# Optimization experiments

Hardware: AMD Instinct MI355X
Metric: run time of the kernel (lower is better)

Reference implementation:

```python
import jax, jax.numpy as jnp
import numpy as np

B, T, C = 8, 2048, 640

def setup_inputs() -> dict:
    key = jax.random.key(0)
    k1, k2, k3, k4 = jax.random.split(key, 4)
    s = 1.0 / np.sqrt(C)  # ~ torch Linear default init scale
    x = jax.random.normal(k1, (B, T, C), dtype=jnp.float32)
    w_q = jax.random.normal(k2, (C, C), dtype=jnp.float32) * s
    w_k = jax.random.normal(k3, (C, C), dtype=jnp.float32) * s
    w_v = jax.random.normal(k4, (C, C), dtype=jnp.float32) * s
    return {"x": x, "w_q": w_q, "w_k": w_k, "w_v": w_v}

def reference(x, w_q, w_k, w_v):
    # nn.Linear computes x @ W.T; weights here stored as (out, in) like torch.
    q = jnp.einsum('btc,oc->bto', x, w_q)
    k = jnp.einsum('btc,oc->bto', x, w_k)
    v = jnp.einsum('btc,oc->bto', x, w_v)
    scale = jnp.sqrt(jnp.asarray(C, dtype=x.dtype))  # note: full n_embd, not per-head
    scores = jnp.einsum('bqc,bkc->bqk', q, k) / scale  # [B,T,T]
    Tn = x.shape[1]
    causal = jnp.triu(jnp.ones((Tn, Tn), dtype=bool), k=1)
    scores = jnp.where(causal[None, :, :], jnp.asarray(-jnp.inf, dtype=x.dtype), scores)
    attn = jax.nn.softmax(scores, axis=-1)
    attn_out = jnp.einsum('bqk,bkc->bqc', attn, v)
    return x + attn_out
```

## Files before the change

kernel.cpp:

```cpp
#include <hip/hip_runtime.h>
#include <stdint.h>
#include <stddef.h>

#define T_SEQ 2048
#define C_DIM 640
#define N_BATCH 8

typedef __bf16 bf16x8 __attribute__((ext_vector_type(8)));
typedef float f32x4 __attribute__((ext_vector_type(4)));

__device__ __forceinline__ unsigned short f2bf(float f) {
  unsigned u = __float_as_uint(f);
  u += 0x7fffu + ((u >> 16) & 1u);
  return (unsigned short)(u >> 16);
}
__device__ __forceinline__ float bf2f(unsigned short h) {
  return __uint_as_float(((unsigned)h) << 16);
}

__device__ __forceinline__ void gll16(const unsigned short* src, unsigned short* dst) {
  __builtin_amdgcn_global_load_lds(
      (const __attribute__((address_space(1))) void*)src,
      (__attribute__((address_space(3))) void*)dst, 16, 0, 0);
}

__device__ __forceinline__ void stage_tile(const unsigned short* gbase, int ldg,
                                           unsigned short* lbuf, int wave, int lane) {
#pragma unroll
  for (int i = 0; i < 4; ++i) {
    const int o   = i * 4096 + wave * 1024 + lane * 16;
    const int row = o >> 7;
    const int cb  = o & 127;
    const int scb = cb ^ ((row & 7) << 4);
    const unsigned short* src = gbase + (size_t)row * ldg + (scb >> 1);
    unsigned short* dst = lbuf + ((i * 4096 + wave * 1024) >> 1);
    gll16(src, dst);
  }
}

__device__ __forceinline__ void tri_decode(int t, int& mi, int& ni) {
  int m = (int)((__fsqrt_rn(8.0f * (float)t + 1.0f) - 1.0f) * 0.5f);
  while ((m + 1) * (m + 2) / 2 <= t) ++m;
  while (m * (m + 1) / 2 > t) --m;
  mi = m;
  ni = t - m * (m + 1) / 2;
}

template <int MODE>
__global__ __launch_bounds__(256) void gemm_k(
    const unsigned short* __restrict__ Abase, const unsigned short* __restrict__ Bbase,
    unsigned short* __restrict__ OutB, float* __restrict__ OutF,
    const float* __restrict__ Lrow, const float* __restrict__ Xres,
    float* __restrict__ Lpart) {
  const int lin = blockIdx.x;
  int mi, ni, bz;
  if constexpr (MODE == 0) {
    const int wg = (lin & 7) * 240 + (lin >> 3);
    mi = wg / 15;
    const int t = wg % 15;
    bz = t / 5;
    ni = t % 5;
  } else if constexpr (MODE == 1) {
    const int wg = (lin & 7) * 136 + (lin >> 3);
    bz = wg / 136;
    tri_decode(wg % 136, mi, ni);
  } else {
    const int wg = (lin & 7) * 80 + (lin >> 3);
    bz = wg / 80;
    const int t = wg % 80;
    mi = 15 - t / 5;
    ni = t % 5;
  }

  __shared__ unsigned short As[2][8192];
  __shared__ unsigned short Bs[2][8192];
  const int tid = threadIdx.x;
  const int wave = tid >> 6, lane = tid & 63;
  const int wm = wave >> 1, wn = wave & 1;

  const unsigned short* Ap;
  const unsigned short* Bp;
  int ldA, ldB, ksteps;
  if constexpr (MODE == 0) {
    Ap = Abase + (size_t)mi * 128 * 640;
    Bp = Bbase + (size_t)bz * 409600 + (size_t)ni * 128 * 640;
    ldA = 640; ldB = 640; ksteps = 10;
  } else if constexpr (MODE == 1) {
    Ap = Abase + (size_t)bz * 1310720 + (size_t)mi * 128 * 640;
    Bp = Bbase + (size_t)bz * 1310720 + (size_t)ni * 128 * 640;
    ldA = 640; ldB = 640; ksteps = 10;
  } else {
    Ap = Abase + (size_t)bz * 4194304 + (size_t)mi * 128 * 2048;
    Bp = Bbase + (size_t)bz * 1310720 + (size_t)ni * 128 * 2048;
    ldA = 2048; ldB = 2048; ksteps = 2 * (mi + 1);
  }

  f32x4 acc[4][4] = {};

  stage_tile(Ap, ldA, As[0], wave, lane);
  stage_tile(Bp, ldB, Bs[0], wave, lane);
  __syncthreads();

  int cur = 0;
  for (int t = 0; t < ksteps; ++t) {
    if (t + 1 < ksteps) {
      stage_tile(Ap + (size_t)(t + 1) * 64, ldA, As[cur ^ 1], wave, lane);
      stage_tile(Bp + (size_t)(t + 1) * 64, ldB, Bs[cur ^ 1], wave, lane);
    }
#pragma unroll
    for (int kk = 0; kk < 2; ++kk) {
      bf16x8 af[4], bfr[4];
#pragma unroll
      for (int mt = 0; mt < 4; ++mt) {
        const int row = wm * 64 + mt * 16 + (lane & 15);
        const int cb  = kk * 64 + ((lane >> 4) << 4);
        af[mt] = *(const bf16x8*)&As[cur][row * 64 + ((cb ^ ((row & 7) << 4)) >> 1)];
      }
#pragma unroll
      for (int nt = 0; nt < 4; ++nt) {
        const int row = wn * 64 + nt * 16 + (lane & 15);
        const int cb  = kk * 64 + ((lane >> 4) << 4);
        bfr[nt] = *(const bf16x8*)&Bs[cur][row * 64 + ((cb ^ ((row & 7) << 4)) >> 1)];
      }
#pragma unroll
      for (int mt = 0; mt < 4; ++mt)
#pragma unroll
        for (int nt = 0; nt < 4; ++nt)
          acc[mt][nt] = __builtin_amdgcn_mfma_f32_16x16x32_bf16(af[mt], bfr[nt],
                                                                acc[mt][nt], 0, 0, 0);
    }
    __syncthreads();
    cur ^= 1;
  }

  if constexpr (MODE == 1) {
#pragma unroll
    for (int mt = 0; mt < 4; ++mt) {
      const int r0 = wm * 64 + mt * 16 + ((lane >> 4) << 2);
      const int grow = mi * 128 + r0;
      float rsum[4] = {0.f, 0.f, 0.f, 0.f};
#pragma unroll
      for (int nt = 0; nt < 4; ++nt) {
        const int gc = ni * 128 + wn * 64 + nt * 16 + (lane & 15);
        const size_t base = (size_t)bz * 4194304 + (size_t)grow * 2048 + gc;
#pragma unroll
        for (int r = 0; r < 4; ++r) {
          const float e = (gc <= grow + r) ? __expf(acc[mt][nt][r]) : 0.0f;
          OutB[base + (size_t)r * 2048] = f2bf(e);
          rsum[r] += e;
        }
      }
#pragma unroll
      for (int off = 1; off < 16; off <<= 1) {
#pragma unroll
        for (int r = 0; r < 4; ++r) rsum[r] += __shfl_xor(rsum[r], off);
      }
      if ((lane & 15) == 0) {
#pragma unroll
        for (int r = 0; r < 4; ++r)
          Lpart[((size_t)bz * 2048 + grow + r) * 32 + ni * 2 + wn] = rsum[r];
      }
    }
  } else {
#pragma unroll
    for (int mt = 0; mt < 4; ++mt) {
#pragma unroll
      for (int nt = 0; nt < 4; ++nt) {
        const int r0 = wm * 64 + mt * 16 + ((lane >> 4) << 2);
        const int c  = wn * 64 + nt * 16 + (lane & 15);
        if constexpr (MODE == 0) {
          const size_t base = (size_t)bz * 10485760 + (size_t)(mi * 128 + r0) * 640 + ni * 128 + c;
#pragma unroll
          for (int r = 0; r < 4; ++r) OutB[base + (size_t)r * 640] = f2bf(acc[mt][nt][r]);
        } else {
          const int grow = mi * 128 + r0;
          const size_t base = (size_t)bz * 1310720 + (size_t)grow * 640 + ni * 128 + c;
#pragma unroll
          for (int r = 0; r < 4; ++r) {
            const float l = Lrow[(size_t)bz * 2048 + grow + r];
            OutF[base + (size_t)r * 640] = acc[mt][nt][r] / l + Xres[base + (size_t)r * 640];
          }
        }
      }
    }
  }
}

__global__ void cast_x_k(const float* __restrict__ x, unsigned short* __restrict__ xb, int n4) {
  const int stride = gridDim.x * blockDim.x;
  for (int i = blockIdx.x * blockDim.x + threadIdx.x; i < n4; i += stride) {
    const float4 v = ((const float4*)x)[i];
    ushort4 o;
    o.x = f2bf(v.x); o.y = f2bf(v.y); o.z = f2bf(v.z); o.w = f2bf(v.w);
    ((ushort4*)xb)[i] = o;
  }
}

__global__ void cast_w_k(const float* __restrict__ wq, const float* __restrict__ wk,
                         const float* __restrict__ wv, unsigned short* __restrict__ wb) {
  const int z = blockIdx.y;
  const float* w = (z == 0) ? wq : ((z == 1) ? wk : wv);
  const float s = (z == 0) ? 0.03952847075210474f : 1.0f;
  const int i = blockIdx.x * 256 + threadIdx.x;
  const float4 v = ((const float4*)w)[i];
  ushort4 o;
  o.x = f2bf(v.x * s); o.y = f2bf(v.y * s); o.z = f2bf(v.z * s); o.w = f2bf(v.w * s);
  ((ushort4*)(wb + (size_t)z * 409600))[i] = o;
}

__global__ void transpose_v(const unsigned short* __restrict__ V,
                            unsigned short* __restrict__ Vt) {
  __shared__ unsigned short tile[32][33];
  const int t0 = blockIdx.x * 32, c0 = blockIdx.y * 32, b = blockIdx.z;
  const unsigned short* Vb = V + (size_t)b * T_SEQ * C_DIM;
  unsigned short* Vtb = Vt + (size_t)b * C_DIM * T_SEQ;
  const int tx = threadIdx.x, ty = threadIdx.y;
#pragma unroll
  for (int i = 0; i < 4; ++i)
    tile[ty + i * 8][tx] = Vb[(size_t)(t0 + ty + i * 8) * C_DIM + c0 + tx];
  __syncthreads();
#pragma unroll
  for (int i = 0; i < 4; ++i)
    Vtb[(size_t)(c0 + ty + i * 8) * T_SEQ + t0 + tx] = tile[tx][ty + i * 8];
}

__global__ void rowsum_k(const float* __restrict__ Lpart, float* __restrict__ Lr) {
  const int i = blockIdx.x * 256 + threadIdx.x;
  const int jmax = (((i & 2047) >> 7) + 1) * 2;
  const float* p = Lpart + (size_t)i * 32;
  float s = 0.f;
  for (int j = 0; j < jmax; ++j) s += p[j];
  Lr[i] = s;
}

extern "C" void kernel_launch(void* const* d_in, const int* in_sizes, int n_in,
                              void* d_out, int out_size, void* d_ws, size_t ws_size,
                              hipStream_t stream) {
  (void)in_sizes; (void)n_in; (void)out_size; (void)ws_size;
  const float* x  = (const float*)d_in[0];
  const float* wq = (const float*)d_in[1];
  const float* wk = (const float*)d_in[2];
  const float* wv = (const float*)d_in[3];
  float* out = (float*)d_out;

  char* ws = (char*)d_ws;
  unsigned short* xb = (unsigned short*)(ws + 0);
  float*          Lpart = (float*)(ws + 0);
  unsigned short* wb = (unsigned short*)(ws + 20971520);
  unsigned short* Qb = (unsigned short*)(ws + 23429120);
  unsigned short* Vt = (unsigned short*)(ws + 86343680);
  float*          Lr = (float*)(ws + 107315200);
  unsigned short* Sb = (unsigned short*)(ws + 107380736);

  cast_x_k<<<2048, 256, 0, stream>>>(x, xb, 2621440);
  cast_w_k<<<dim3(400, 3), 256, 0, stream>>>(wq, wk, wv, wb);
  gemm_k<0><<<1920, 256, 0, stream>>>(xb, wb, Qb, nullptr, nullptr, nullptr, nullptr);
  transpose_v<<<dim3(64, 20, 8), dim3(32, 8), 0, stream>>>(Qb + (size_t)2 * 10485760, Vt);
  gemm_k<1><<<1088, 256, 0, stream>>>(Qb, Qb + 10485760, Sb, nullptr, nullptr, nullptr,
                                      Lpart);
  rowsum_k<<<64, 256, 0, stream>>>(Lpart, Lr);
  gemm_k<2><<<640, 256, 0, stream>>>(Sb, Vt, nullptr, out, Lr, x, nullptr);
}
```

Measured before the change: 164.0 us.

## Fold Wq and Wk into one matrix and write V transposed from projection

Precomputes M = Wk^T·(Wq/scale) with a split-K GEMM and reduction, so only y = x·M and V are projected instead of Q, K and V. Scores are then computed as y·x^T, removing one full projection GEMM. The V projection stores its output transposed directly, eliminating the separate transpose kernel. The residual add now reads bf16 x instead of fp32 x, which slightly lowers precision.

Result: faster. 152.9 us (-6.7%).

```diff
diff --git a/kernel.cpp b/kernel.cpp
--- a/kernel.cpp
+++ b/kernel.cpp
@@ -49,27 +49,33 @@
 template <int MODE>
 __global__ __launch_bounds__(256) void gemm_k(
     const unsigned short* __restrict__ Abase, const unsigned short* __restrict__ Bbase,
-    unsigned short* __restrict__ OutB, float* __restrict__ OutF,
-    const float* __restrict__ Lrow, const float* __restrict__ Xres,
+    const unsigned short* __restrict__ B2base, unsigned short* __restrict__ OutB,
+    unsigned short* __restrict__ OutB2, float* __restrict__ OutF,
+    const float* __restrict__ Lrow, const unsigned short* __restrict__ Xres,
     float* __restrict__ Lpart) {
   const int lin = blockIdx.x;
   int mi, ni, bz;
   if constexpr (MODE == 0) {
-    const int wg = (lin & 7) * 240 + (lin >> 3);
-    mi = wg / 15;
-    const int t = wg % 15;
+    const int wg = (lin & 7) * 160 + (lin >> 3);
+    mi = wg / 10;
+    const int t = wg % 10;
     bz = t / 5;
     ni = t % 5;
   } else if constexpr (MODE == 1) {
     const int wg = (lin & 7) * 136 + (lin >> 3);
     bz = wg / 136;
     tri_decode(wg % 136, mi, ni);
-  } else {
+  } else if constexpr (MODE == 2) {
     const int wg = (lin & 7) * 80 + (lin >> 3);
     bz = wg / 80;
     const int t = wg % 80;
     mi = 15 - t / 5;
     ni = t % 5;
+  } else {
+    bz = lin / 25;
+    const int rem = lin % 25;
+    mi = rem / 5;
+    ni = rem % 5;
   }
 
   __shared__ unsigned short As[2][8192];
@@ -82,17 +88,21 @@
   const unsigned short* Bp;
   int ldA, ldB, ksteps;
   if constexpr (MODE == 0) {
-    Ap = Abase + (size_t)mi * 128 * 640;
-    Bp = Bbase + (size_t)bz * 409600 + (size_t)ni * 128 * 640;
+    Ap = Abase + (size_t)mi * 81920;
+    Bp = ((bz == 0) ? Bbase : B2base) + (size_t)ni * 81920;
     ldA = 640; ldB = 640; ksteps = 10;
   } else if constexpr (MODE == 1) {
-    Ap = Abase + (size_t)bz * 1310720 + (size_t)mi * 128 * 640;
-    Bp = Bbase + (size_t)bz * 1310720 + (size_t)ni * 128 * 640;
+    Ap = Abase + (size_t)bz * 1310720 + (size_t)mi * 81920;
+    Bp = Bbase + (size_t)bz * 1310720 + (size_t)ni * 81920;
     ldA = 640; ldB = 640; ksteps = 10;
+  } else if constexpr (MODE == 2) {
+    Ap = Abase + (size_t)bz * 4194304 + (size_t)mi * 262144;
+    Bp = Bbase + (size_t)bz * 1310720 + (size_t)ni * 262144;
+    ldA = 2048; ldB = 2048; ksteps = 2 * (mi + 1);
   } else {
-    Ap = Abase + (size_t)bz * 4194304 + (size_t)mi * 128 * 2048;
-    Bp = Bbase + (size_t)bz * 1310720 + (size_t)ni * 128 * 2048;
-    ldA = 2048; ldB = 2048; ksteps = 2 * (mi + 1);
+    Ap = Abase + (size_t)mi * 81920 + bz * 128;
+    Bp = Bbase + (size_t)ni * 81920 + bz * 128;
+    ldA = 640; ldB = 640; ksteps = 2;
   }
 
   f32x4 acc[4][4] = {};
@@ -169,17 +179,32 @@
         const int r0 = wm * 64 + mt * 16 + ((lane >> 4) << 2);
         const int c  = wn * 64 + nt * 16 + (lane & 15);
         if constexpr (MODE == 0) {
-          const size_t base = (size_t)bz * 10485760 + (size_t)(mi * 128 + r0) * 640 + ni * 128 + c;
-#pragma unroll
-          for (int r = 0; r < 4; ++r) OutB[base + (size_t)r * 640] = f2bf(acc[mt][nt][r]);
-        } else {
+          if (bz == 0) {
+            const size_t base = (size_t)(mi * 128 + r0) * 640 + ni * 128 + c;
+#pragma unroll
+            for (int r = 0; r < 4; ++r) OutB[base + (size_t)r * 640] = f2bf(acc[mt][nt][r]);
+          } else {
+            const int b = mi >> 4;
+            const int tloc = ((mi & 15) << 7) + r0;
+            const int gc = ni * 128 + c;
+            ushort4 o4;
+            o4.x = f2bf(acc[mt][nt][0]); o4.y = f2bf(acc[mt][nt][1]);
+            o4.z = f2bf(acc[mt][nt][2]); o4.w = f2bf(acc[mt][nt][3]);
+            *(ushort4*)&OutB2[(size_t)b * 1310720 + (size_t)gc * 2048 + tloc] = o4;
+          }
+        } else if constexpr (MODE == 2) {
           const int grow = mi * 128 + r0;
           const size_t base = (size_t)bz * 1310720 + (size_t)grow * 640 + ni * 128 + c;
 #pragma unroll
           for (int r = 0; r < 4; ++r) {
             const float l = Lrow[(size_t)bz * 2048 + grow + r];
-            OutF[base + (size_t)r * 640] = acc[mt][nt][r] / l + Xres[base + (size_t)r * 640];
+            OutF[base + (size_t)r * 640] =
+                acc[mt][nt][r] / l + bf2f(Xres[base + (size_t)r * 640]);
           }
+        } else {
+          const size_t base = (size_t)bz * 409600 + (size_t)(mi * 128 + r0) * 640 + ni * 128 + c;
+#pragma unroll
+          for (int r = 0; r < 4; ++r) OutF[base + (size_t)r * 640] = acc[mt][nt][r];
         }
       }
     }
@@ -196,32 +221,44 @@
   }
 }
 
-__global__ void cast_w_k(const float* __restrict__ wq, const float* __restrict__ wk,
-                         const float* __restrict__ wv, unsigned short* __restrict__ wb) {
+__global__ void tcast_w(const float* __restrict__ wq, const float* __restrict__ wk,
+                        const float* __restrict__ wv, unsigned short* __restrict__ wqT,
+                        unsigned short* __restrict__ wkT, unsigned short* __restrict__ wvb) {
   const int z = blockIdx.y;
-  const float* w = (z == 0) ? wq : ((z == 1) ? wk : wv);
+  const int tx = threadIdx.x, ty = threadIdx.y;
+  if (z == 2) {
+    const int e = (blockIdx.x * 256 + ty * 32 + tx) * 4;
+    const float4 v = *(const float4*)&wv[e];
+    ushort4 o;
+    o.x = f2bf(v.x); o.y = f2bf(v.y); o.z = f2bf(v.z); o.w = f2bf(v.w);
+    *(ushort4*)&wvb[e] = o;
+    return;
+  }
+  __shared__ float tile[32][33];
+  const float* w = (z == 0) ? wq : wk;
+  unsigned short* wT = (z == 0) ? wqT : wkT;
   const float s = (z == 0) ? 0.03952847075210474f : 1.0f;
-  const int i = blockIdx.x * 256 + threadIdx.x;
-  const float4 v = ((const float4*)w)[i];
+  const int bo = (blockIdx.x / 20) * 32, bc = (blockIdx.x % 20) * 32;
+#pragma unroll
+  for (int i = 0; i < 4; ++i)
+    tile[ty + i * 8][tx] = w[(size_t)(bo + ty + i * 8) * 640 + bc + tx];
+  __syncthreads();
+#pragma unroll
+  for (int i = 0; i < 4; ++i)
+    wT[(size_t)(bc + ty + i * 8) * 640 + bo + tx] = f2bf(tile[tx][ty + i * 8] * s);
+}
+
+__global__ void reduce_mt(const float* __restrict__ Mpart, unsigned short* __restrict__ Mt) {
+  const int e = (blockIdx.x * 256 + threadIdx.x) * 4;
+  float4 a = *(const float4*)&Mpart[e];
+#pragma unroll
+  for (int p = 1; p < 5; ++p) {
+    const float4 b = *(const float4*)&Mpart[(size_t)p * 409600 + e];
+    a.x += b.x; a.y += b.y; a.z += b.z; a.w += b.w;
+  }
   ushort4 o;
-  o.x = f2bf(v.x * s); o.y = f2bf(v.y * s); o.z = f2bf(v.z * s); o.w = f2bf(v.w * s);
-  ((ushort4*)(wb + (size_t)z * 409600))[i] = o;
-}
-
-__global__ void transpose_v(const unsigned short* __restrict__ V,
-                            unsigned short* __restrict__ Vt) {
-  __shared__ unsigned short tile[32][33];
-  const int t0 = blockIdx.x * 32, c0 = blockIdx.y * 32, b = blockIdx.z;
-  const unsigned short* Vb = V + (size_t)b * T_SEQ * C_DIM;
-  unsigned short* Vtb = Vt + (size_t)b * C_DIM * T_SEQ;
-  const int tx = threadIdx.x, ty = threadIdx.y;
-#pragma unroll
-  for (int i = 0; i < 4; ++i)
-    tile[ty + i * 8][tx] = Vb[(size_t)(t0 + ty + i * 8) * C_DIM + c0 + tx];
-  __syncthreads();
-#pragma unroll
-  for (int i = 0; i < 4; ++i)
-    Vtb[(size_t)(c0 + ty + i * 8) * T_SEQ + t0 + tx] = tile[tx][ty + i * 8];
+  o.x = f2bf(a.x); o.y = f2bf(a.y); o.z = f2bf(a.z); o.w = f2bf(a.w);
+  *(ushort4*)&Mt[e] = o;
 }
 
 __global__ void rowsum_k(const float* __restrict__ Lpart, float* __restrict__ Lr) {
@@ -244,20 +281,28 @@
   float* out = (float*)d_out;
 
   char* ws = (char*)d_ws;
-  unsigned short* xb = (unsigned short*)(ws + 0);
-  float*          Lpart = (float*)(ws + 0);
-  unsigned short* wb = (unsigned short*)(ws + 20971520);
-  unsigned short* Qb = (unsigned short*)(ws + 23429120);
-  unsigned short* Vt = (unsigned short*)(ws + 86343680);
-  float*          Lr = (float*)(ws + 107315200);
-  unsigned short* Sb = (unsigned short*)(ws + 107380736);
+  unsigned short* xb  = (unsigned short*)(ws + 0);
+  unsigned short* wqT = (unsigned short*)(ws + 20971520);
+  unsigned short* wkT = (unsigned short*)(ws + 21790720);
+  unsigned short* wvb = (unsigned short*)(ws + 22609920);
+  unsigned short* Mt  = (unsigned short*)(ws + 23429120);
+  unsigned short* y   = (unsigned short*)(ws + 24248320);
+  unsigned short* Vt  = (unsigned short*)(ws + 45219840);
+  float*          Mpart = (float*)(ws + 66191360);
+  float*          Lpart = (float*)(ws + 74383360);
+  float*          Lr  = (float*)(ws + 76480512);
+  unsigned short* Sb  = (unsigned short*)(ws + 76546048);
 
   cast_x_k<<<2048, 256, 0, stream>>>(x, xb, 2621440);
-  cast_w_k<<<dim3(400, 3), 256, 0, stream>>>(wq, wk, wv, wb);
-  gemm_k<0><<<1920, 256, 0, stream>>>(xb, wb, Qb, nullptr, nullptr, nullptr, nullptr);
-  transpose_v<<<dim3(64, 20, 8), dim3(32, 8), 0, stream>>>(Qb + (size_t)2 * 10485760, Vt);
-  gemm_k<1><<<1088, 256, 0, stream>>>(Qb, Qb + 10485760, Sb, nullptr, nullptr, nullptr,
-                                      Lpart);
+  tcast_w<<<dim3(400, 3), dim3(32, 8), 0, stream>>>(wq, wk, wv, wqT, wkT, wvb);
+  gemm_k<3><<<125, 256, 0, stream>>>(wkT, wqT, nullptr, nullptr, nullptr, Mpart,
+                                     nullptr, nullptr, nullptr);
+  reduce_mt<<<400, 256, 0, stream>>>(Mpart, Mt);
+  gemm_k<0><<<1280, 256, 0, stream>>>(xb, Mt, wvb, y, Vt, nullptr, nullptr, nullptr,
+                                      nullptr);
+  gemm_k<1><<<1088, 256, 0, stream>>>(y, xb, nullptr, Sb, nullptr, nullptr, nullptr,
+                                      nullptr, Lpart);
   rowsum_k<<<64, 256, 0, stream>>>(Lpart, Lr);
-  gemm_k<2><<<640, 256, 0, stream>>>(Sb, Vt, nullptr, out, Lr, x, nullptr);
-}
+  gemm_k<2><<<640, 256, 0, stream>>>(Sb, Vt, nullptr, nullptr, nullptr, out, Lr, xb,
+                                     nullptr);
+}
```
